# Optimization experiments

Hardware: AMD Instinct MI355X
Metric: run time of the kernel (lower is better)

## Reference

```python
import jax, jax.numpy as jnp
import numpy as np

N = 4096          # num_nodes
E = 131072        # num_edges
DIN = 1024        # in_features
D = 1024          # out_features
H = 8             # num_heads
DH = D // H       # head_dim
T = 4             # num_edge_types
SELF_LOOP_IDX = 3


def setup_inputs() -> dict:
    key = jax.random.key(0)
    ks = jax.random.split(key, 16)
    s = 0.02
    x = jax.random.normal(ks[0], (N, DIN), dtype=jnp.float32)
    edge_index = jax.random.randint(ks[1], (2, E), 0, N)
    edge_type = jax.random.randint(ks[2], (E,), 1, T + 1)  # values in 1..T
    return {
        "x": x,
        "edge_index": edge_index,
        "edge_type": edge_type,
        "edge_type_weights": jnp.ones((T,), dtype=jnp.float32),
        "Wq": jax.random.normal(ks[3], (D, DIN)) * s,
        "bq": jnp.zeros((D,), jnp.float32),
        "Wk": jax.random.normal(ks[4], (D, DIN)) * s,
        "bk": jnp.zeros((D,), jnp.float32),
        "Wv": jax.random.normal(ks[5], (D, DIN)) * s,
        "bv": jnp.zeros((D,), jnp.float32),
        "in_proj_w": jax.random.normal(ks[6], (3 * D, D)) * s,
        "in_proj_b": jnp.zeros((3 * D,), jnp.float32),
        "out_w": jax.random.normal(ks[7], (D, D)) * s,
        "out_b": jnp.zeros((D,), jnp.float32),
    }


def _build_mask(edge_index, edge_type, edge_type_weights):
    # Vectorized form of the original Python edge loop:
    # attn_mask[src, dst] = softplus(w[edge_type - 1]); missing self-loops get softplus(w[3]).
    w_soft = jax.nn.softplus(edge_type_weights)          # [T]
    src, dst = edge_index[0], edge_index[1]
    mask = jnp.full((N, N), -jnp.inf, dtype=jnp.float32)
    mask = mask.at[src, dst].set(w_soft[edge_type - 1])
    idx = jnp.arange(N)
    diag = mask[idx, idx]
    diag = jnp.where(jnp.isfinite(diag), diag, w_soft[SELF_LOOP_IDX])
    return mask.at[idx, idx].set(diag)


def reference(x, edge_index, edge_type, edge_type_weights,
              Wq, bq, Wk, bk, Wv, bv, in_proj_w, in_proj_b, out_w, out_b):
    # Outer projections (the module's own q/k/v Linear layers)
    q = x @ Wq.T + bq
    k = x @ Wk.T + bk
    v = x @ Wv.T + bv

    attn_mask = _build_mask(edge_index, edge_type, edge_type_weights)  # [N, N]

    # nn.MultiheadAttention internal projections
    wq2, wk2, wv2 = in_proj_w[:D], in_proj_w[D:2 * D], in_proj_w[2 * D:]
    bq2, bk2, bv2 = in_proj_b[:D], in_proj_b[D:2 * D], in_proj_b[2 * D:]
    Qh = (q @ wq2.T + bq2).reshape(N, H, DH).transpose(1, 0, 2)  # [H, N, DH]
    Kh = (k @ wk2.T + bk2).reshape(N, H, DH).transpose(1, 0, 2)
    Vh = (v @ wv2.T + bv2).reshape(N, H, DH).transpose(1, 0, 2)

    scale = 1.0 / jnp.sqrt(jnp.float32(DH))
    scores = jnp.einsum('hnd,hmd->hnm', Qh * scale, Kh) + attn_mask[None]  # [H, N, N]
    attn = jax.nn.softmax(scores, axis=-1)
    ctx = jnp.einsum('hnm,hmd->hnd', attn, Vh)                              # [H, N, DH]
    ctx = ctx.transpose(1, 0, 2).reshape(N, D)
    out = ctx @ out_w.T + out_b                                             # [N, D]

    attn_weights = attn.mean(axis=0)[None]  # averaged over heads, [1, N, N]
    return out, attn_weights, attn_mask
```

## Files before the change

kernel.cpp:

```cpp
#include <hip/hip_runtime.h>
#include <hip/hip_bf16.h>
#include <cstddef>

#define N 4096
#define E_EDGES 131072
#define DIN 1024
#define D 1024
#define H 8
#define DH 128
#define MAXNBR 192

#define NEG_BIG -3.0e38f

typedef unsigned short u16;
typedef unsigned int u32;
typedef __attribute__((ext_vector_type(8))) short bh8;
typedef __attribute__((ext_vector_type(4))) float f32x4;

__device__ __forceinline__ float softplusf(float x) {
    return fmaxf(x, 0.f) + log1pf(__expf(-fabsf(x)));
}

__device__ __forceinline__ u16 f2bf(float f) {
    u32 u = __float_as_uint(f);
    u += 0x7FFFu + ((u >> 16) & 1u);
    return (u16)(u >> 16);
}

__device__ __forceinline__ float bflo(u32 u) { return __uint_as_float(u << 16); }
__device__ __forceinline__ float bfhi(u32 u) { return __uint_as_float(u & 0xFFFF0000u); }

__global__ void fill_kernel(float* __restrict__ attn_w, float* __restrict__ mask) {
    size_t i = ((size_t)blockIdx.x * 256 + threadIdx.x) * 4;
    const size_t total = (size_t)N * N;
    const size_t stride = (size_t)gridDim.x * 256 * 4;
    const float4 z = make_float4(0.f, 0.f, 0.f, 0.f);
    const float4 ni = make_float4(NEG_BIG, NEG_BIG, NEG_BIG, NEG_BIG);
    for (; i < total; i += stride) {
        *reinterpret_cast<float4*>(attn_w + i) = z;
        *reinterpret_cast<float4*>(mask + i) = ni;
    }
}

__global__ void scatter_kernel(const int* __restrict__ ei, const int* __restrict__ et,
                               const float* __restrict__ etw, float* __restrict__ mask) {
    int e = blockIdx.x * 256 + threadIdx.x;
    if (e >= E_EDGES) return;
    int s = ei[e];
    int d = ei[E_EDGES + e];
    float w = softplusf(etw[et[e] - 1]);
    mask[(size_t)s * N + d] = w;
}

__global__ void diag_kernel(const float* __restrict__ etw, float* __restrict__ mask) {
    int i = blockIdx.x * 256 + threadIdx.x;
    if (i >= N) return;
    float w = softplusf(etw[3]);
    size_t p = (size_t)i * N + i;
    float cur = mask[p];
    if (!(cur > -1e37f)) mask[p] = w;
}

__global__ void build_nbr_kernel(const float* __restrict__ mask,
                                 int* __restrict__ nbr_idx, int* __restrict__ nbr_cnt) {
    const int row = blockIdx.x;
    const int lane = threadIdx.x;
    const float* mrow = mask + (size_t)row * N;
    int cnt = 0;
    for (int base = 0; base < N; base += 64) {
        float v = mrow[base + lane];
        bool fin = (v > -1e37f);
        unsigned long long bal = __ballot(fin);
        int pre = __popcll(bal & ((1ull << lane) - 1ull));
        if (fin) {
            int slot = cnt + pre;
            if (slot < MAXNBR) nbr_idx[(size_t)row * MAXNBR + slot] = base + lane;
        }
        cnt += __popcll(bal);
    }
    if (lane == 0) nbr_cnt[row] = cnt < MAXNBR ? cnt : MAXNBR;
}

__global__ void convert_hi_kernel(const float* __restrict__ in,
                                  u16* __restrict__ hi, int n) {
    int i = (blockIdx.x * 256 + threadIdx.x) * 4;
    const int stride = gridDim.x * 256 * 4;
    for (; i < n; i += stride) {
        float4 f = *reinterpret_cast<const float4*>(in + i);
        ushort4 hv;
        hv.x = f2bf(f.x); hv.y = f2bf(f.y);
        hv.z = f2bf(f.z); hv.w = f2bf(f.w);
        *reinterpret_cast<ushort4*>(hi + i) = hv;
    }
}

__global__ void transpose_hi_kernel(const float* __restrict__ Wq,
                                    const float* __restrict__ Wk,
                                    const float* __restrict__ Wv,
                                    u16* __restrict__ WTh) {
    __shared__ float t[32][33];
    const int z = blockIdx.z;
    const float* src = (z == 0) ? Wq : (z == 1) ? Wk : Wv;
    u16* th = WTh + (size_t)z * D * DIN;
    const int tx = threadIdx.x, ty = threadIdx.y;
    const int k0 = blockIdx.y * 32, n0 = blockIdx.x * 32;
#pragma unroll
    for (int i = 0; i < 4; ++i)
        t[ty + 8 * i][tx] = src[(size_t)(k0 + ty + 8 * i) * DIN + n0 + tx];
    __syncthreads();
#pragma unroll
    for (int i = 0; i < 4; ++i) {
        float v = t[tx][ty + 8 * i];
        th[(size_t)(n0 + ty + 8 * i) * D + k0 + tx] = f2bf(v);
    }
}

__global__ __launch_bounds__(256) void beff_kernel(
    const float* __restrict__ ipw, const float* __restrict__ ipb,
    const float* __restrict__ bq, const float* __restrict__ bk,
    const float* __restrict__ bv, float* __restrict__ beff) {
    const int o = blockIdx.x * 4 + (threadIdx.x >> 6);
    const int lane = threadIdx.x & 63;
    const int p = o >> 10;
    const float* b = (p == 0) ? bq : (p == 1) ? bk : bv;
    const float* wrow = ipw + (size_t)o * D;
    float s = 0.f;
#pragma unroll
    for (int k = lane * 4; k < D; k += 256) {
        float4 w4 = *reinterpret_cast<const float4*>(wrow + k);
        float4 b4 = *reinterpret_cast<const float4*>(b + k);
        s += w4.x * b4.x + w4.y * b4.y + w4.z * b4.z + w4.w * b4.w;
    }
#pragma unroll
    for (int off = 32; off >= 1; off >>= 1) s += __shfl_xor(s, off);
    if (lane == 0) beff[o] = s + ipb[o];
}

#define BM 128
#define BN 128
#define BK 32

template <int MODE, int NZ>
__global__ __launch_bounds__(256) void gemm_h(
    const u16* __restrict__ Ah, size_t sA,
    const u16* __restrict__ Bh, size_t sB,
    const float* __restrict__ bias, int sBias,
    float* __restrict__ Cf, u16* __restrict__ Ch, size_t sC,
    int M, int Nn, int K) {
    __shared__ u16 smem[2][2][BM * BK];
    const int bid = blockIdx.x;
    const int bx = bid & 7;
    const int r = bid >> 3;
    const int z = r % NZ;
    const int by = r / NZ;
    Ah += (size_t)z * sA;
    Bh += (size_t)z * sB;
    if (bias) bias += (size_t)z * sBias;

    const int tid = threadIdx.x;
    const int wave = tid >> 6, lane = tid & 63;
    const int m0 = by * BM, n0 = bx * BN;
    const int wm = (wave >> 1) * 64, wn = (wave & 1) * 64;
    const int lr = lane & 15, lc = lane >> 4;

    const u16* gsrc = (wave < 2) ? Ah : Bh;
    const int row0 = ((wave < 2) ? m0 : n0) + (wave & 1) * 64;
    const int srow = lane >> 2;
    const int scol = (lane & 3) * 8;
    const u16* gbase = gsrc + (size_t)(row0 + srow) * K + scol;
    const int ldst = (wave & 1) * 2048;

    f32x4 acc[4][4] = {};
    const int NT = K / BK;

#pragma unroll
    for (int i = 0; i < 4; ++i) {
        __builtin_amdgcn_global_load_lds(
            (const __attribute__((address_space(1))) void*)(gbase + (size_t)i * 16 * K),
            (__attribute__((address_space(3))) void*)(&smem[0][wave >> 1][ldst + i * 512]),
            16, 0, 0);
    }
    __syncthreads();

    int cur = 0;
    for (int t = 0; t < NT; ++t) {
        if (t + 1 < NT) {
            const u16* gnext = gbase + (size_t)(t + 1) * BK;
#pragma unroll
            for (int i = 0; i < 4; ++i) {
                __builtin_amdgcn_global_load_lds(
                    (const __attribute__((address_space(1))) void*)(gnext + (size_t)i * 16 * K),
                    (__attribute__((address_space(3))) void*)(&smem[cur ^ 1][wave >> 1][ldst + i * 512]),
                    16, 0, 0);
            }
        }
        const u16* sA = smem[cur][0];
        const u16* sB = smem[cur][1];
        bh8 a[4], b[4];
#pragma unroll
        for (int i = 0; i < 4; ++i) {
            a[i] = *reinterpret_cast<const bh8*>(sA + (wm + i * 16 + lr) * BK + lc * 8);
            b[i] = *reinterpret_cast<const bh8*>(sB + (wn + i * 16 + lr) * BK + lc * 8);
        }
#pragma unroll
        for (int i = 0; i < 4; ++i)
#pragma unroll
            for (int j = 0; j < 4; ++j)
                acc[i][j] = __builtin_amdgcn_mfma_f32_16x16x32_bf16(a[i], b[j], acc[i][j], 0, 0, 0);
        __syncthreads();
        cur ^= 1;
    }

    const int orow = m0 + wm + lc * 4;
    const int ocol0 = n0 + wn + lr;
#pragma unroll
    for (int j = 0; j < 4; ++j) {
        const int col = ocol0 + j * 16;
        const float bb = bias ? bias[col] : 0.0f;
#pragma unroll
        for (int i = 0; i < 4; ++i)
#pragma unroll
            for (int r2 = 0; r2 < 4; ++r2) {
                const int row = orow + i * 16 + r2;
                const float v = acc[i][j][r2] + bb;
                if (MODE == 0) {
                    (Ch + (size_t)z * sC)[(size_t)row * Nn + col] = f2bf(v);
                } else {
                    if (z == 0) {
                        Cf[(size_t)row * Nn + col] = v;
                    } else {
                        (Ch + (size_t)(z - 1) * sC)[(size_t)row * Nn + col] = f2bf(v);
                    }
                }
            }
    }
}

__global__ __launch_bounds__(512) void attn_kernel(
    const float* __restrict__ Q, const u16* __restrict__ Kb, const u16* __restrict__ Vb,
    const int* __restrict__ nbr_idx, const int* __restrict__ nbr_cnt,
    const float* __restrict__ mask, float* __restrict__ attn_w,
    u16* __restrict__ ctx_h) {
    const int n = blockIdx.x;
    const int tid = threadIdx.x;
    const int lane = tid & 63;
    const int wave = tid >> 6;
    const int grp = lane >> 4;
    const int gi = lane & 15;
    __shared__ int s_col[MAXNBR];
    __shared__ float s_mv[MAXNBR];
    __shared__ float s_s[H][MAXNBR];
    __shared__ float s_p[H][MAXNBR];
    const int cnt = nbr_cnt[n];
    for (int j = tid; j < cnt; j += 512) {
        int c = nbr_idx[(size_t)n * MAXNBR + j];
        s_col[j] = c;
        s_mv[j] = mask[(size_t)n * N + c];
    }
    __syncthreads();

    const float* qp = Q + (size_t)n * D + wave * DH + gi * 8;
    const float4 qa = *reinterpret_cast<const float4*>(qp);
    const float4 qb = *reinterpret_cast<const float4*>(qp + 4);
    const float scale = 0.08838834764831845f;
    const size_t hoff = (size_t)wave * DH + gi * 8;

    auto dot8 = [&](uint4 k) {
        float s = qa.x * bflo(k.x) + qa.y * bfhi(k.x);
        s += qa.z * bflo(k.y) + qa.w * bfhi(k.y);
        s += qb.x * bflo(k.z) + qb.y * bfhi(k.z);
        s += qb.z * bflo(k.w) + qb.w * bfhi(k.w);
        return s;
    };

    for (int base = 0; base < cnt; base += 8) {
        const int j0 = base + grp, j1 = base + 4 + grp;
        const int jc0 = (j0 < cnt) ? j0 : cnt - 1;
        const int jc1 = (j1 < cnt) ? j1 : cnt - 1;
        uint4 k0 = *reinterpret_cast<const uint4*>(Kb + (size_t)s_col[jc0] * D + hoff);
        uint4 k1 = *reinterpret_cast<const uint4*>(Kb + (size_t)s_col[jc1] * D + hoff);
        float d0 = dot8(k0);
        float d1 = dot8(k1);
#pragma unroll
        for (int off = 1; off <= 8; off <<= 1) {
            d0 += __shfl_xor(d0, off);
            d1 += __shfl_xor(d1, off);
        }
        if (gi == 0) {
            if (j0 < cnt) s_s[wave][j0] = d0 * scale + s_mv[j0];
            if (j1 < cnt) s_s[wave][j1] = d1 * scale + s_mv[j1];
        }
    }

    float sv0 = (lane < cnt) ? s_s[wave][lane] : -INFINITY;
    float sv1 = (64 + lane < cnt) ? s_s[wave][64 + lane] : -INFINITY;
    float sv2 = (128 + lane < cnt) ? s_s[wave][128 + lane] : -INFINITY;
    float m = fmaxf(sv0, fmaxf(sv1, sv2));
#pragma unroll
    for (int off = 32; off >= 1; off >>= 1) m = fmaxf(m, __shfl_xor(m, off));
    float e0 = __expf(sv0 - m), e1 = __expf(sv1 - m), e2 = __expf(sv2 - m);
    float l = e0 + e1 + e2;
#pragma unroll
    for (int off = 32; off >= 1; off >>= 1) l += __shfl_xor(l, off);
    float inv = 1.0f / l;
    if (lane < cnt) s_p[wave][lane] = e0 * inv;
    if (64 + lane < cnt) s_p[wave][64 + lane] = e1 * inv;
    if (128 + lane < cnt) s_p[wave][128 + lane] = e2 * inv;

    float c[8] = {};
    for (int base = 0; base < cnt; base += 8) {
        const int j0 = base + grp, j1 = base + 4 + grp;
        const bool a0 = j0 < cnt, a1 = j1 < cnt;
        const int jc0 = a0 ? j0 : cnt - 1;
        const int jc1 = a1 ? j1 : cnt - 1;
        const float p0 = a0 ? s_p[wave][j0] : 0.f;
        const float p1 = a1 ? s_p[wave][j1] : 0.f;
        uint4 v0 = *reinterpret_cast<const uint4*>(Vb + (size_t)s_col[jc0] * D + hoff);
        uint4 v1 = *reinterpret_cast<const uint4*>(Vb + (size_t)s_col[jc1] * D + hoff);
        c[0] += p0 * bflo(v0.x) + p1 * bflo(v1.x);
        c[1] += p0 * bfhi(v0.x) + p1 * bfhi(v1.x);
        c[2] += p0 * bflo(v0.y) + p1 * bflo(v1.y);
        c[3] += p0 * bfhi(v0.y) + p1 * bfhi(v1.y);
        c[4] += p0 * bflo(v0.z) + p1 * bflo(v1.z);
        c[5] += p0 * bfhi(v0.z) + p1 * bfhi(v1.z);
        c[6] += p0 * bflo(v0.w) + p1 * bflo(v1.w);
        c[7] += p0 * bfhi(v0.w) + p1 * bfhi(v1.w);
    }
#pragma unroll
    for (int k = 0; k < 8; ++k) {
        c[k] += __shfl_xor(c[k], 16);
        c[k] += __shfl_xor(c[k], 32);
    }
    if (grp == 0) {
        uint4 ph;
        ph.x = (u32)f2bf(c[0]) | ((u32)f2bf(c[1]) << 16);
        ph.y = (u32)f2bf(c[2]) | ((u32)f2bf(c[3]) << 16);
        ph.z = (u32)f2bf(c[4]) | ((u32)f2bf(c[5]) << 16);
        ph.w = (u32)f2bf(c[6]) | ((u32)f2bf(c[7]) << 16);
        *reinterpret_cast<uint4*>(ctx_h + (size_t)n * D + hoff) = ph;
    }

    __syncthreads();
    for (int q = tid; q < cnt; q += 512) {
        float s = 0.f;
#pragma unroll
        for (int h = 0; h < H; ++h) s += s_p[h][q];
        attn_w[(size_t)n * N + s_col[q]] = s * 0.125f;
    }
}

extern "C" void kernel_launch(void* const* d_in, const int* in_sizes, int n_in,
                              void* d_out, int out_size, void* d_ws, size_t ws_size,
                              hipStream_t stream) {
    const float* x = (const float*)d_in[0];
    const int* ei = (const int*)d_in[1];
    const int* et = (const int*)d_in[2];
    const float* etw = (const float*)d_in[3];
    const float* Wq = (const float*)d_in[4];
    const float* bq = (const float*)d_in[5];
    const float* Wk = (const float*)d_in[6];
    const float* bk = (const float*)d_in[7];
    const float* Wv = (const float*)d_in[8];
    const float* bv = (const float*)d_in[9];
    const float* ipw = (const float*)d_in[10];
    const float* ipb = (const float*)d_in[11];
    const float* ow = (const float*)d_in[12];
    const float* ob = (const float*)d_in[13];

    float* out = (float*)d_out;
    float* attn_w = out + (size_t)N * D;
    float* mask = attn_w + (size_t)N * N;

    u16* x_h = (u16*)d_ws;
    u16* W2h = x_h + (size_t)N * DIN;
    u16* OWh = W2h + (size_t)3 * D * D;
    u16* WTh = OWh + (size_t)D * D;
    u16* WEh = WTh + (size_t)3 * D * DIN;
    float* Qf = (float*)(WEh + (size_t)3 * D * DIN);
    u16* Kb16 = (u16*)(Qf + (size_t)N * D);
    u16* Vb16 = Kb16 + (size_t)N * D;
    float* beff = (float*)(Vb16 + (size_t)N * D);
    int* nbr_idx = (int*)(beff + 3 * D);
    int* nbr_cnt = nbr_idx + (size_t)N * MAXNBR;
    u16* ctx_h = WTh;

    fill_kernel<<<2048, 256, 0, stream>>>(attn_w, mask);
    scatter_kernel<<<(E_EDGES + 255) / 256, 256, 0, stream>>>(ei, et, etw, mask);
    diag_kernel<<<(N + 255) / 256, 256, 0, stream>>>(etw, mask);
    build_nbr_kernel<<<N, 64, 0, stream>>>(mask, nbr_idx, nbr_cnt);

    convert_hi_kernel<<<2048, 256, 0, stream>>>(x, x_h, N * DIN);
    convert_hi_kernel<<<1024, 256, 0, stream>>>(ipw, W2h, 3 * D * D);
    convert_hi_kernel<<<512, 256, 0, stream>>>(ow, OWh, D * D);
    {
        dim3 tg(DIN / 32, D / 32, 3);
        transpose_hi_kernel<<<tg, dim3(32, 8), 0, stream>>>(Wq, Wk, Wv, WTh);
    }
    beff_kernel<<<768, 256, 0, stream>>>(ipw, ipb, bq, bk, bv, beff);

    gemm_h<0, 3><<<192, 256, 0, stream>>>(
        W2h, (size_t)D * D, WTh, (size_t)D * DIN,
        nullptr, 0, nullptr, WEh, (size_t)D * DIN, D, DIN, D);

    gemm_h<1, 3><<<768, 256, 0, stream>>>(
        x_h, (size_t)0, WEh, (size_t)D * DIN,
        beff, D, Qf, Kb16, (size_t)N * D, N, D, DIN);

    attn_kernel<<<N, 512, 0, stream>>>(Qf, Kb16, Vb16, nbr_idx, nbr_cnt,
                                       mask, attn_w, ctx_h);

    gemm_h<1, 1><<<256, 256, 0, stream>>>(
        ctx_h, (size_t)0, OWh, (size_t)0,
        ob, 0, out, nullptr, (size_t)0, N, D, D);
}
```

Measured before the change: 409.8 us.

## Triple-buffer GEMM LDS staging with prefetch distance two and partial vmcnt waits

Moves the bf16 GEMM mainloop from double to triple LDS buffering. Each iteration now prefetches tile t+2 and waits only until the older tile's loads have landed (vmcnt(4)) before the barrier, instead of draining all loads with __syncthreads. The goal is to hide more global-load latency behind the MFMA work. In exchange, LDS use rises to 48KB per block, which can lower occupancy, and the hand-written waitcnt logic depends on the exact count of outstanding loads.

```diff
diff --git a/kernel.cpp b/kernel.cpp
--- a/kernel.cpp
+++ b/kernel.cpp
@@ -147,7 +147,7 @@
     const float* __restrict__ bias, int sBias,
     float* __restrict__ Cf, u16* __restrict__ Ch, size_t sC,
     int M, int Nn, int K) {
-    __shared__ u16 smem[2][2][BM * BK];
+    __shared__ u16 smem[3][2][BM * BK];
     const int bid = blockIdx.x;
     const int bx = bid & 7;
     const int r = bid >> 3;
@@ -168,32 +168,35 @@
     const int srow = lane >> 2;
     const int scol = (lane & 3) * 8;
     const u16* gbase = gsrc + (size_t)(row0 + srow) * K + scol;
+    const int tsel = wave >> 1;
     const int ldst = (wave & 1) * 2048;
+
+    auto stage = [&](int t, int buf) {
+        const u16* g = gbase + (size_t)t * BK;
+#pragma unroll
+        for (int i = 0; i < 4; ++i) {
+            __builtin_amdgcn_global_load_lds(
+                (const __attribute__((address_space(1))) void*)(g + (size_t)i * 16 * K),
+                (__attribute__((address_space(3))) void*)(&smem[buf][tsel][ldst + i * 512]),
+                16, 0, 0);
+        }
+    };
 
     f32x4 acc[4][4] = {};
     const int NT = K / BK;
 
-#pragma unroll
-    for (int i = 0; i < 4; ++i) {
-        __builtin_amdgcn_global_load_lds(
-            (const __attribute__((address_space(1))) void*)(gbase + (size_t)i * 16 * K),
-            (__attribute__((address_space(3))) void*)(&smem[0][wave >> 1][ldst + i * 512]),
-            16, 0, 0);
-    }
-    __syncthreads();
+    stage(0, 0);
+    stage(1, 1);
+    asm volatile("s_waitcnt vmcnt(4)" ::: "memory");
+    __builtin_amdgcn_sched_barrier(0);
+    __builtin_amdgcn_s_barrier();
+    __builtin_amdgcn_sched_barrier(0);
 
     int cur = 0;
     for (int t = 0; t < NT; ++t) {
-        if (t + 1 < NT) {
-            const u16* gnext = gbase + (size_t)(t + 1) * BK;
-#pragma unroll
-            for (int i = 0; i < 4; ++i) {
-                __builtin_amdgcn_global_load_lds(
-                    (const __attribute__((address_space(1))) void*)(gnext + (size_t)i * 16 * K),
-                    (__attribute__((address_space(3))) void*)(&smem[cur ^ 1][wave >> 1][ldst + i * 512]),
-                    16, 0, 0);
-            }
-        }
+        const bool pf = (t + 2 < NT);
+        if (pf) stage(t + 2, (cur + 2) % 3);
+
         const u16* sA = smem[cur][0];
         const u16* sB = smem[cur][1];
         bh8 a[4], b[4];
@@ -207,8 +210,16 @@
 #pragma unroll
             for (int j = 0; j < 4; ++j)
                 acc[i][j] = __builtin_amdgcn_mfma_f32_16x16x32_bf16(a[i], b[j], acc[i][j], 0, 0, 0);
-        __syncthreads();
-        cur ^= 1;
+
+        if (pf) {
+            asm volatile("s_waitcnt vmcnt(4)" ::: "memory");
+        } else {
+            asm volatile("s_waitcnt vmcnt(0)" ::: "memory");
+        }
+        __builtin_amdgcn_sched_barrier(0);
+        __builtin_amdgcn_s_barrier();
+        __builtin_amdgcn_sched_barrier(0);
+        cur = (cur + 1) % 3;
     }
 
     const int orow = m0 + wm + lc * 4;
```

New measurement: 398.6 us. 1.03x faster.
